# Kernel optimization log

Hardware: AMD Instinct MI355X
Metric: run time of the kernel (lower is better)

## Reference

```python
import jax, jax.numpy as jnp
import numpy as np

P, B, A, NBT, NC, NTAB, G = 512, 512, 32, 40, 3, 40, 36
NA = B * A


def setup_inputs() -> dict:
    key = jax.random.key(0)
    rng = np.random.default_rng(0)
    coords = jax.random.normal(key, (P, NA, 3), dtype=jnp.float32) * 3.0
    # residue b occupies atoms [b*A, (b+1)*A)
    offsets = np.broadcast_to(np.arange(B, dtype=np.int32) * A, (P, B)).copy()
    block_type = rng.integers(0, NBT, size=(P, B)).astype(np.int32)
    # simple linear chain per pose: conn 0 = lower (prev residue), conn 1 = upper (next residue)
    inter = np.full((P, B, NC, 2), -1, dtype=np.int32)
    inter[:, 1:, 0, 0] = np.arange(B - 1, dtype=np.int32)
    inter[:, 1:, 0, 1] = 1
    inter[:, :-1, 1, 0] = np.arange(1, B, dtype=np.int32)
    inter[:, :-1, 1, 1] = 0
    down = rng.integers(0, A, size=(NBT, NC, A)).astype(np.int32)
    bt_rama_table = rng.integers(0, NTAB, size=(NBT, 2)).astype(np.int32)
    bt_upper_conn_ind = np.ones(NBT, dtype=np.int32)
    bt_is_pro = rng.integers(0, 2, size=NBT).astype(np.int32)
    # unresolved torsion atoms: (local_atom_ind, conn_ind, n_bonds_from_conn); atom_ind<0 => via connection
    tor = np.zeros((NBT, 8, 3), dtype=np.int32)
    tor[:, 0] = (-1, 0, 0)  # phi: prev-C via lower conn
    tor[:, 1] = (0, -1, 0)  # N
    tor[:, 2] = (1, -1, 0)  # CA
    tor[:, 3] = (2, -1, 0)  # C
    tor[:, 4] = (0, -1, 0)  # psi: N
    tor[:, 5] = (1, -1, 0)  # CA
    tor[:, 6] = (2, -1, 0)  # C
    tor[:, 7] = (-1, 1, 0)  # next-N via upper conn
    rama_tables = jax.random.normal(jax.random.fold_in(key, 1), (NTAB, G, G), dtype=jnp.float32)
    tp = np.zeros((NTAB, 2, 2), dtype=np.float32)
    tp[:, 0, :] = -np.pi            # bb start
    tp[:, 1, :] = 2.0 * np.pi / G   # bb step
    return dict(
        coords=coords,
        pose_stack_block_coord_offset=jnp.asarray(offsets),
        pose_stack_block_type=jnp.asarray(block_type),
        pose_stack_inter_residue_connections=jnp.asarray(inter),
        bt_atom_downstream_of_conn=jnp.asarray(down),
        bt_rama_table=jnp.asarray(bt_rama_table),
        bt_upper_conn_ind=jnp.asarray(bt_upper_conn_ind),
        bt_is_pro=jnp.asarray(bt_is_pro),
        bt_rama_torsion_atoms=jnp.asarray(tor),
        rama_tables=rama_tables,
        table_params=jnp.asarray(tp),
    )


def _dihedral(p):
    # p: [..., 4, 3] -> dihedral angle [...] via atan2 formulation
    b1 = p[..., 1, :] - p[..., 0, :]
    b2 = p[..., 2, :] - p[..., 1, :]
    b3 = p[..., 3, :] - p[..., 2, :]
    n1 = jnp.cross(b1, b2)
    n2 = jnp.cross(b2, b3)
    b2n = b2 / (jnp.linalg.norm(b2, axis=-1, keepdims=True) + 1e-12)
    m1 = jnp.cross(n1, b2n)
    x = jnp.sum(n1 * n2, axis=-1)
    y = jnp.sum(m1 * n2, axis=-1)
    return jnp.arctan2(y, x)


def _catmull_rom_w(f):
    # weights over 4 neighbors (i-1, i, i+1, i+2); f in [0,1)
    f2 = f * f
    f3 = f2 * f
    return jnp.stack(
        [0.5 * (-f3 + 2 * f2 - f), 0.5 * (3 * f3 - 5 * f2 + 2),
         0.5 * (-3 * f3 + 4 * f2 + f), 0.5 * (f3 - f2)], axis=-1)


def reference(coords, pose_stack_block_coord_offset, pose_stack_block_type,
              pose_stack_inter_residue_connections, bt_atom_downstream_of_conn,
              bt_rama_table, bt_upper_conn_ind, bt_is_pro, bt_rama_torsion_atoms,
              rama_tables, table_params):
    nP, nB = pose_stack_block_type.shape
    nG = rama_tables.shape[-1]
    pidx = jnp.arange(nP)[:, None, None]
    bidx = jnp.arange(nB)[None, :, None]
    bt = pose_stack_block_type                       # [P,B]
    tor = bt_rama_torsion_atoms[bt]                  # [P,B,8,3]
    atom_ind, conn_ind, nbonds = tor[..., 0], tor[..., 1], tor[..., 2]
    safe_conn = jnp.clip(conn_ind, 0, None)
    other_block = pose_stack_inter_residue_connections[pidx, bidx, safe_conn, 0]  # [P,B,8]
    other_conn = pose_stack_inter_residue_connections[pidx, bidx, safe_conn, 1]
    conn_ok = (conn_ind >= 0) & (other_block >= 0)
    ob = jnp.clip(other_block, 0, None)
    oc = jnp.clip(other_conn, 0, None)
    obt = bt[pidx, ob]                               # [P,B,8]
    down_atom = bt_atom_downstream_of_conn[obt, oc, nbonds]
    conn_global = pose_stack_block_coord_offset[pidx, ob] + down_atom
    local_global = pose_stack_block_coord_offset[pidx, bidx] + jnp.clip(atom_ind, 0, None)
    use_local = atom_ind >= 0
    gidx = jnp.where(use_local, local_global, conn_global)  # [P,B,8]
    atom_ok = use_local | conn_ok
    xyz = coords[pidx, gidx]                         # [P,B,8,3]
    ang = _dihedral(xyz.reshape(nP, nB, 2, 4, 3))    # [P,B,2] -> (phi, psi)
    tor_ok = jnp.all(atom_ok.reshape(nP, nB, 2, 4), axis=-1)
    # table selection: proline-dependent on the NEXT residue
    uc = bt_upper_conn_ind[bt]                       # [P,B]
    p2 = jnp.arange(nP)[:, None]
    b2 = jnp.arange(nB)[None, :]
    nb = pose_stack_inter_residue_connections[p2, b2, uc, 0]  # [P,B]
    nb_ok = nb >= 0
    nbt = bt[p2, jnp.clip(nb, 0, None)]
    tab = bt_rama_table[bt, bt_is_pro[nbt]]          # [P,B]
    start = table_params[tab, 0]                     # [P,B,2]
    step = table_params[tab, 1]
    u = (ang - start) / step                         # [P,B,2]
    i0f = jnp.floor(u)
    f = u - i0f
    i0 = i0f.astype(jnp.int32)
    offs = jnp.arange(-1, 3, dtype=jnp.int32)        # 4 spline neighbors
    ii = jnp.mod(i0[..., 0:1] + offs, nG)            # [P,B,4] periodic phi bins
    jj = jnp.mod(i0[..., 1:2] + offs, nG)            # [P,B,4] periodic psi bins
    wphi = _catmull_rom_w(f[..., 0])                 # [P,B,4]
    wpsi = _catmull_rom_w(f[..., 1])
    vals = rama_tables[tab[..., None, None], ii[..., :, None], jj[..., None, :]]  # [P,B,4,4]
    e = jnp.einsum('pbi,pbj,pbij->pb', wphi, wpsi, vals)
    ok = tor_ok[..., 0] & tor_ok[..., 1] & nb_ok
    return jnp.sum(jnp.where(ok, e, 0.0), axis=-1)   # [P] per-pose rama score
```

## Files before the change

### kernel.cpp

```cpp
#include <hip/hip_runtime.h>
#include <math.h>

#define NP 512
#define NBLK 512
#define NA_ 32
#define NCn 3
#define NG 36
#define NBT 40
#define NTAB 40

struct F3 { float x, y, z; };
__device__ inline F3 f3sub(F3 a, F3 b) { return {a.x - b.x, a.y - b.y, a.z - b.z}; }
__device__ inline F3 f3cross(F3 a, F3 b) {
    return {a.y * b.z - a.z * b.y, a.z * b.x - a.x * b.z, a.x * b.y - a.y * b.x};
}
__device__ inline float f3dot(F3 a, F3 b) { return a.x * b.x + a.y * b.y + a.z * b.z; }

__global__ __launch_bounds__(NBLK) void rama_kernel(
    const float* __restrict__ coords,
    const int*   __restrict__ offsets,
    const int*   __restrict__ block_type,
    const int*   __restrict__ inter,
    const int*   __restrict__ down,
    const int*   __restrict__ bt_rama_table,
    const int*   __restrict__ bt_upper_conn,
    const int*   __restrict__ bt_is_pro,
    const int*   __restrict__ tor_atoms,
    const float* __restrict__ rama_tables,
    const float* __restrict__ table_params,
    float*       __restrict__ out)
{
    __shared__ int   s_bt[NBLK];
    __shared__ int   s_off[NBLK];
    __shared__ int   s_inter[NBLK * NCn * 2];
    __shared__ int   s_tor[NBT * 8 * 3];
    __shared__ int   s_down[NBT * NCn * NA_];
    __shared__ int   s_rt[NBT * 2];
    __shared__ int   s_uc[NBT];
    __shared__ int   s_pro[NBT];
    __shared__ float s_tp[NTAB * 4];
    __shared__ float partial[NBLK / 64];

    const int p   = blockIdx.x;
    const int tid = threadIdx.x;

    s_bt[tid]  = block_type[p * NBLK + tid];
    s_off[tid] = offsets[p * NBLK + tid];
    #pragma unroll
    for (int i = tid; i < NBLK * NCn * 2; i += NBLK)
        s_inter[i] = inter[p * NBLK * NCn * 2 + i];
    for (int i = tid; i < NBT * 24; i += NBLK)  s_tor[i]  = tor_atoms[i];
    for (int i = tid; i < NBT * NCn * NA_; i += NBLK) s_down[i] = down[i];
    if (tid < NBT * 2)  s_rt[tid]  = bt_rama_table[tid];
    if (tid < NBT)      { s_uc[tid] = bt_upper_conn[tid]; s_pro[tid] = bt_is_pro[tid]; }
    if (tid < NTAB * 4) s_tp[tid]  = table_params[tid];
    __syncthreads();

    const int b     = tid;
    const int bt    = s_bt[b];
    const int off_b = s_off[b];
    const float* pose_coords = coords + (size_t)p * NBLK * NA_ * 3;

    int  g[8];
    bool ok[8];
    #pragma unroll
    for (int k = 0; k < 8; ++k) {
        const int ti       = (bt * 8 + k) * 3;
        const int atom_ind = s_tor[ti + 0];
        const int conn_ind = s_tor[ti + 1];
        const int nbonds   = s_tor[ti + 2];
        if (atom_ind >= 0) {
            g[k]  = off_b + atom_ind;
            ok[k] = true;
        } else {
            const int sc  = conn_ind > 0 ? conn_ind : 0;
            const int ib  = (b * NCn + sc) * 2;
            const int ob  = s_inter[ib + 0];
            const int oc  = s_inter[ib + 1];
            ok[k] = (conn_ind >= 0) && (ob >= 0);
            const int obc = ob > 0 ? ob : 0;
            const int occ = oc > 0 ? oc : 0;
            const int obt = s_bt[obc];
            g[k] = s_off[obc] + s_down[(obt * NCn + occ) * NA_ + nbonds];
        }
    }

    const int uc    = s_uc[bt];
    const int nb    = s_inter[(b * NCn + uc) * 2 + 0];
    const bool nbok = nb >= 0;
    const int nbc   = nb > 0 ? nb : 0;
    const int tab   = s_rt[bt * 2 + s_pro[s_bt[nbc]]];

    F3 pts[8];
    #pragma unroll
    for (int k = 0; k < 8; ++k) {
        const float* c = pose_coords + (size_t)g[k] * 3;
        pts[k] = {c[0], c[1], c[2]};
    }

    float ang[2];
    #pragma unroll
    for (int t = 0; t < 2; ++t) {
        const F3* q = pts + t * 4;
        const F3 b1 = f3sub(q[1], q[0]);
        const F3 b2 = f3sub(q[2], q[1]);
        const F3 b3 = f3sub(q[3], q[2]);
        const F3 n1 = f3cross(b1, b2);
        const F3 n2 = f3cross(b2, b3);
        const float inv = 1.0f / (sqrtf(f3dot(b2, b2)) + 1e-12f);
        const F3 b2n = {b2.x * inv, b2.y * inv, b2.z * inv};
        const F3 m1  = f3cross(n1, b2n);
        ang[t] = atan2f(f3dot(m1, n2), f3dot(n1, n2));
    }

    const bool all_ok = ok[0] & ok[1] & ok[2] & ok[3] & ok[4] & ok[5] & ok[6] & ok[7] & nbok;

    float e = 0.0f;
    if (all_ok) {
        float w0[4], w1[4];
        int   ii[4], jj[4];
        #pragma unroll
        for (int d = 0; d < 2; ++d) {
            const float start = s_tp[tab * 4 + d];
            const float step  = s_tp[tab * 4 + 2 + d];
            const float u   = (ang[d] - start) / step;
            const float i0f = floorf(u);
            const float f   = u - i0f;
            const int   i0  = (int)i0f;
            const float f2 = f * f, f3v = f2 * f;
            float* w = (d == 0) ? w0 : w1;
            w[0] = 0.5f * (-f3v + 2.0f * f2 - f);
            w[1] = 0.5f * (3.0f * f3v - 5.0f * f2 + 2.0f);
            w[2] = 0.5f * (-3.0f * f3v + 4.0f * f2 + f);
            w[3] = 0.5f * (f3v - f2);
            int* idx = (d == 0) ? ii : jj;
            #pragma unroll
            for (int k = 0; k < 4; ++k) {
                int v = (i0 - 1 + k) % NG;
                if (v < 0) v += NG;
                idx[k] = v;
            }
        }
        const float* T = rama_tables + (size_t)tab * NG * NG;
        #pragma unroll
        for (int i = 0; i < 4; ++i) {
            const float* Tr = T + ii[i] * NG;
            float rowsum = 0.0f;
            #pragma unroll
            for (int j = 0; j < 4; ++j) rowsum += w1[j] * Tr[jj[j]];
            e += w0[i] * rowsum;
        }
    }

    float v = e;
    #pragma unroll
    for (int o = 32; o > 0; o >>= 1) v += __shfl_down(v, o);
    const int wave = tid >> 6;
    const int lane = tid & 63;
    if (lane == 0) partial[wave] = v;
    __syncthreads();
    if (tid == 0) {
        float s = 0.0f;
        #pragma unroll
        for (int i = 0; i < NBLK / 64; ++i) s += partial[i];
        out[p] = s;
    }
}

extern "C" void kernel_launch(void* const* d_in, const int* in_sizes, int n_in,
                              void* d_out, int out_size, void* d_ws, size_t ws_size,
                              hipStream_t stream) {
    (void)in_sizes; (void)n_in; (void)out_size; (void)d_ws; (void)ws_size;
    rama_kernel<<<NP, NBLK, 0, stream>>>(
        (const float*)d_in[0],
        (const int*)d_in[1],
        (const int*)d_in[2],
        (const int*)d_in[3],
        (const int*)d_in[4],
        (const int*)d_in[5],
        (const int*)d_in[6],
        (const int*)d_in[7],
        (const int*)d_in[8],
        (const float*)d_in[9],
        (const float*)d_in[10],
        (float*)d_out);
}
```

Before: 173.2 us.

## Split each residue across two threads, one per torsion angle

Doubles the block to 1024 threads so each residue is handled by a pair of lanes. Each lane gathers four atoms and computes one dihedral, and the pair swaps angles and validity flags through __shfl_xor. Each lane then evaluates two of the four spline rows. The goal is more parallelism and memory-level parallelism for the scattered coordinate gathers. The cost is some duplicated setup per pair, a larger block, and a higher register-pressure target from launch bounds of 8.

Measured after the change: 173.0 us. About the same (-0.1%).

```diff
diff --git a/kernel.cpp b/kernel.cpp
--- a/kernel.cpp
+++ b/kernel.cpp
@@ -3,6 +3,7 @@
 
 #define NP 512
 #define NBLK 512
+#define NTHREADS 1024
 #define NA_ 32
 #define NCn 3
 #define NG 36
@@ -16,7 +17,7 @@
 }
 __device__ inline float f3dot(F3 a, F3 b) { return a.x * b.x + a.y * b.y + a.z * b.z; }
 
-__global__ __launch_bounds__(NBLK) void rama_kernel(
+__global__ __launch_bounds__(NTHREADS, 8) void rama_kernel(
     const float* __restrict__ coords,
     const int*   __restrict__ offsets,
     const int*   __restrict__ block_type,
@@ -33,57 +34,81 @@
     __shared__ int   s_bt[NBLK];
     __shared__ int   s_off[NBLK];
     __shared__ int   s_inter[NBLK * NCn * 2];
-    __shared__ int   s_tor[NBT * 8 * 3];
+    __shared__ int   s_tor[NBT * 24];
     __shared__ int   s_down[NBT * NCn * NA_];
     __shared__ int   s_rt[NBT * 2];
     __shared__ int   s_uc[NBT];
     __shared__ int   s_pro[NBT];
     __shared__ float s_tp[NTAB * 4];
-    __shared__ float partial[NBLK / 64];
+    __shared__ float partial[NTHREADS / 64];
 
     const int p   = blockIdx.x;
     const int tid = threadIdx.x;
 
-    s_bt[tid]  = block_type[p * NBLK + tid];
-    s_off[tid] = offsets[p * NBLK + tid];
-    #pragma unroll
-    for (int i = tid; i < NBLK * NCn * 2; i += NBLK)
+    if (tid < NBLK) {
+        s_bt[tid]  = block_type[p * NBLK + tid];
+        s_off[tid] = offsets[p * NBLK + tid];
+    }
+    for (int i = tid; i < NBLK * NCn * 2; i += NTHREADS)
         s_inter[i] = inter[p * NBLK * NCn * 2 + i];
-    for (int i = tid; i < NBT * 24; i += NBLK)  s_tor[i]  = tor_atoms[i];
-    for (int i = tid; i < NBT * NCn * NA_; i += NBLK) s_down[i] = down[i];
-    if (tid < NBT * 2)  s_rt[tid]  = bt_rama_table[tid];
+    for (int i = tid; i < NBT * 24; i += NTHREADS)        s_tor[i]  = tor_atoms[i];
+    for (int i = tid; i < NBT * NCn * NA_; i += NTHREADS) s_down[i] = down[i];
+    if (tid < NBT * 2)  s_rt[tid] = bt_rama_table[tid];
     if (tid < NBT)      { s_uc[tid] = bt_upper_conn[tid]; s_pro[tid] = bt_is_pro[tid]; }
-    if (tid < NTAB * 4) s_tp[tid]  = table_params[tid];
+    if (tid < NTAB * 4) s_tp[tid] = table_params[tid];
     __syncthreads();
 
-    const int b     = tid;
-    const int bt    = s_bt[b];
+    const int b  = tid >> 1;
+    const int t  = tid & 1;
+    const int bt = s_bt[b];
     const int off_b = s_off[b];
     const float* pose_coords = coords + (size_t)p * NBLK * NA_ * 3;
 
-    int  g[8];
-    bool ok[8];
+    int  g[4];
+    bool ok4 = true;
     #pragma unroll
-    for (int k = 0; k < 8; ++k) {
-        const int ti       = (bt * 8 + k) * 3;
+    for (int a = 0; a < 4; ++a) {
+        const int ti       = (bt * 8 + t * 4 + a) * 3;
         const int atom_ind = s_tor[ti + 0];
         const int conn_ind = s_tor[ti + 1];
         const int nbonds   = s_tor[ti + 2];
         if (atom_ind >= 0) {
-            g[k]  = off_b + atom_ind;
-            ok[k] = true;
+            g[a] = off_b + atom_ind;
         } else {
             const int sc  = conn_ind > 0 ? conn_ind : 0;
             const int ib  = (b * NCn + sc) * 2;
             const int ob  = s_inter[ib + 0];
             const int oc  = s_inter[ib + 1];
-            ok[k] = (conn_ind >= 0) && (ob >= 0);
+            ok4 = ok4 && (conn_ind >= 0) && (ob >= 0);
             const int obc = ob > 0 ? ob : 0;
             const int occ = oc > 0 ? oc : 0;
             const int obt = s_bt[obc];
-            g[k] = s_off[obc] + s_down[(obt * NCn + occ) * NA_ + nbonds];
+            g[a] = s_off[obc] + s_down[(obt * NCn + occ) * NA_ + nbonds];
         }
     }
+
+    F3 pts[4];
+    #pragma unroll
+    for (int a = 0; a < 4; ++a) {
+        const float* c = pose_coords + (size_t)g[a] * 3;
+        pts[a] = {c[0], c[1], c[2]};
+    }
+
+    const F3 b1 = f3sub(pts[1], pts[0]);
+    const F3 b2 = f3sub(pts[2], pts[1]);
+    const F3 b3 = f3sub(pts[3], pts[2]);
+    const F3 n1 = f3cross(b1, b2);
+    const F3 n2 = f3cross(b2, b3);
+    const float inv = 1.0f / (sqrtf(f3dot(b2, b2)) + 1e-12f);
+    const F3 b2n = {b2.x * inv, b2.y * inv, b2.z * inv};
+    const F3 m1  = f3cross(n1, b2n);
+    const float ang = atan2f(f3dot(m1, n2), f3dot(n1, n2));
+
+    const float ang_o = __shfl_xor(ang, 1);
+    const int   oki   = ok4 ? 1 : 0;
+    const int   ok_o  = __shfl_xor(oki, 1);
+    const float phi = (t == 0) ? ang   : ang_o;
+    const float psi = (t == 0) ? ang_o : ang;
 
     const int uc    = s_uc[bt];
     const int nb    = s_inter[(b * NCn + uc) * 2 + 0];
@@ -91,44 +116,21 @@
     const int nbc   = nb > 0 ? nb : 0;
     const int tab   = s_rt[bt * 2 + s_pro[s_bt[nbc]]];
 
-    F3 pts[8];
-    #pragma unroll
-    for (int k = 0; k < 8; ++k) {
-        const float* c = pose_coords + (size_t)g[k] * 3;
-        pts[k] = {c[0], c[1], c[2]};
-    }
-
-    float ang[2];
-    #pragma unroll
-    for (int t = 0; t < 2; ++t) {
-        const F3* q = pts + t * 4;
-        const F3 b1 = f3sub(q[1], q[0]);
-        const F3 b2 = f3sub(q[2], q[1]);
-        const F3 b3 = f3sub(q[3], q[2]);
-        const F3 n1 = f3cross(b1, b2);
-        const F3 n2 = f3cross(b2, b3);
-        const float inv = 1.0f / (sqrtf(f3dot(b2, b2)) + 1e-12f);
-        const F3 b2n = {b2.x * inv, b2.y * inv, b2.z * inv};
-        const F3 m1  = f3cross(n1, b2n);
-        ang[t] = atan2f(f3dot(m1, n2), f3dot(n1, n2));
-    }
-
-    const bool all_ok = ok[0] & ok[1] & ok[2] & ok[3] & ok[4] & ok[5] & ok[6] & ok[7] & nbok;
-
     float e = 0.0f;
-    if (all_ok) {
-        float w0[4], w1[4];
+    if (oki && ok_o && nbok) {
+        float wphi[4], wpsi[4];
         int   ii[4], jj[4];
         #pragma unroll
         for (int d = 0; d < 2; ++d) {
+            const float a0    = (d == 0) ? phi : psi;
             const float start = s_tp[tab * 4 + d];
             const float step  = s_tp[tab * 4 + 2 + d];
-            const float u   = (ang[d] - start) / step;
+            const float u   = (a0 - start) / step;
             const float i0f = floorf(u);
             const float f   = u - i0f;
             const int   i0  = (int)i0f;
             const float f2 = f * f, f3v = f2 * f;
-            float* w = (d == 0) ? w0 : w1;
+            float* w = (d == 0) ? wphi : wpsi;
             w[0] = 0.5f * (-f3v + 2.0f * f2 - f);
             w[1] = 0.5f * (3.0f * f3v - 5.0f * f2 + 2.0f);
             w[2] = 0.5f * (-3.0f * f3v + 4.0f * f2 + f);
@@ -143,12 +145,13 @@
         }
         const float* T = rama_tables + (size_t)tab * NG * NG;
         #pragma unroll
-        for (int i = 0; i < 4; ++i) {
+        for (int r = 0; r < 2; ++r) {
+            const int i = 2 * t + r;
             const float* Tr = T + ii[i] * NG;
             float rowsum = 0.0f;
             #pragma unroll
-            for (int j = 0; j < 4; ++j) rowsum += w1[j] * Tr[jj[j]];
-            e += w0[i] * rowsum;
+            for (int j = 0; j < 4; ++j) rowsum += wpsi[j] * Tr[jj[j]];
+            e += wphi[i] * rowsum;
         }
     }
 
@@ -162,7 +165,7 @@
     if (tid == 0) {
         float s = 0.0f;
         #pragma unroll
-        for (int i = 0; i < NBLK / 64; ++i) s += partial[i];
+        for (int i = 0; i < NTHREADS / 64; ++i) s += partial[i];
         out[p] = s;
     }
 }
@@ -171,7 +174,7 @@
                               void* d_out, int out_size, void* d_ws, size_t ws_size,
                               hipStream_t stream) {
     (void)in_sizes; (void)n_in; (void)out_size; (void)d_ws; (void)ws_size;
-    rama_kernel<<<NP, NBLK, 0, stream>>>(
+    rama_kernel<<<NP, NTHREADS, 0, stream>>>(
         (const float*)d_in[0],
         (const int*)d_in[1],
         (const int*)d_in[2],
```
